# Kernel optimization log

Hardware: AMD Instinct MI355X
Metric: run time of the kernel (lower is better)

The kernel has to match this reference:

```python
import jax, jax.numpy as jnp
import numpy as np

N_NODES = 100000
N_EDGES = 1600000
D_IN = 128
D_HID = 128
N_CLS = 16
N_GRAPHS = 64


def setup_inputs() -> dict:
    key = jax.random.key(0)
    ks = jax.random.split(key, 12)
    h = jax.random.normal(ks[0], (N_NODES, D_IN), dtype=jnp.float32)
    src = jax.random.randint(ks[1], (N_EDGES,), 0, N_NODES, dtype=jnp.int32)
    dst = jax.random.randint(ks[2], (N_EDGES,), 0, N_NODES, dtype=jnp.int32)
    graph_ids = jnp.sort(jax.random.randint(ks[3], (N_NODES,), 0, N_GRAPHS, dtype=jnp.int32))
    s = 1.0 / np.sqrt(D_IN)
    W1_self = jax.random.uniform(ks[4], (D_IN, D_HID), jnp.float32, -s, s)
    W1_neigh = jax.random.uniform(ks[5], (D_IN, D_HID), jnp.float32, -s, s)
    b1 = jnp.zeros((D_HID,), jnp.float32)
    s2 = 1.0 / np.sqrt(D_HID)
    W2_self = jax.random.uniform(ks[6], (D_HID, D_HID), jnp.float32, -s2, s2)
    W2_neigh = jax.random.uniform(ks[7], (D_HID, D_HID), jnp.float32, -s2, s2)
    b2 = jnp.zeros((D_HID,), jnp.float32)
    Wc = jax.random.uniform(ks[8], (D_HID, N_CLS), jnp.float32, -s2, s2)
    bc = jnp.zeros((N_CLS,), jnp.float32)
    return {"h": h, "src": src, "dst": dst, "graph_ids": graph_ids, "num_graphs": N_GRAPHS,
            "W1_self": W1_self, "W1_neigh": W1_neigh, "b1": b1,
            "W2_self": W2_self, "W2_neigh": W2_neigh, "b2": b2,
            "Wc": Wc, "bc": bc}


def _sage_conv(h, src, dst, W_self, W_neigh, b):
    # DGL SAGEConv 'mean': out = fc_self(h) + fc_neigh(mean of in-neighbor feats) + bias
    n = h.shape[0]
    msg = jnp.take(h, src, axis=0)                               # [E, d] gather
    agg = jax.ops.segment_sum(msg, dst, num_segments=n)          # [N, d] scatter-add
    deg = jax.ops.segment_sum(jnp.ones((src.shape[0],), h.dtype), dst, num_segments=n)
    neigh = agg / jnp.maximum(deg, 1.0)[:, None]                 # mean, zero-degree safe
    return h @ W_self + neigh @ W_neigh + b


def reference(h, src, dst, graph_ids, num_graphs,
              W1_self, W1_neigh, b1, W2_self, W2_neigh, b2, Wc, bc):
    x = jax.nn.relu(_sage_conv(h, src, dst, W1_self, W1_neigh, b1))
    x = _sage_conv(x, src, dst, W2_self, W2_neigh, b2)
    # dgl.mean_nodes: per-graph mean over node features
    gsum = jax.ops.segment_sum(x, graph_ids, num_segments=num_graphs)    # [G, d]
    gcnt = jax.ops.segment_sum(jnp.ones((x.shape[0],), x.dtype), graph_ids, num_segments=num_graphs)
    hg = gsum / jnp.maximum(gcnt, 1.0)[:, None]
    return hg @ Wc + bc                                                  # [G, num_classes]
```

## Files before the change

### kernel.cpp

```cpp
#include <hip/hip_runtime.h>

#define D        128
#define N_GRAPHS 64
#define N_CLS    16
#define LDA      40
#define SLOTS    48
#define CAP      8192

typedef unsigned int   uint;
typedef unsigned short ushort;
typedef __attribute__((ext_vector_type(8))) short short8;
typedef __attribute__((ext_vector_type(4))) float f32x4;

__device__ inline ushort f2b(float f) {
    uint u = __float_as_uint(f);
    u += 0x7fffu + ((u >> 16) & 1u);
    return (ushort)(u >> 16);
}


__global__ __launch_bounds__(256) void k_part(
    const int* __restrict__ src, const int* __restrict__ dst,
    int* __restrict__ bcount, uint* __restrict__ ebuf, int E, int NB) {
    __shared__ int hist[512], base[512], lcur[512];
    int t = threadIdx.x;
    int per = (E + gridDim.x - 1) / gridDim.x;
    int e0 = blockIdx.x * per;
    int e1 = min(e0 + per, E);
    for (int i = t; i < NB; i += 256) { hist[i] = 0; lcur[i] = 0; }
    __syncthreads();
    for (int e = e0 + t; e < e1; e += 256) atomicAdd(&hist[dst[e] >> 8], 1);
    __syncthreads();
    for (int i = t; i < NB; i += 256)
        base[i] = hist[i] ? atomicAdd(&bcount[i], hist[i]) : 0;
    __syncthreads();
    for (int e = e0 + t; e < e1; e += 256) {
        int dd = dst[e];
        int b = dd >> 8;
        int off = atomicAdd(&lcur[b], 1);
        int pos = base[b] + off;
        if (pos < CAP)
            ebuf[(size_t)b * CAP + pos] = ((uint)src[e] << 8) | (uint)(dd & 255);
    }
}


__global__ __launch_bounds__(1024) void k_bucket(
    const uint* __restrict__ ebuf, const int* __restrict__ bcount,
    int* __restrict__ csrf, int* __restrict__ deg, float* __restrict__ invdeg,
    int N) {
    __shared__ int ldeg[256];
    __shared__ int lcsr[256 * SLOTS];
    int b = blockIdx.x, t = threadIdx.x;
    if (t < 256) ldeg[t] = 0;
    __syncthreads();
    int cnt = bcount[b];
    if (cnt > CAP) cnt = CAP;
    const uint* __restrict__ eb = ebuf + (size_t)b * CAP;
    for (int i = t; i < cnt; i += 1024) {
        uint r = eb[i];
        int dl = r & 255;
        int sl = atomicAdd(&ldeg[dl], 1);
        if (sl < SLOTS) lcsr[dl * SLOTS + sl] = (int)(r >> 8);
    }
    __syncthreads();
    int n0 = b << 8;
    int lim = (N - n0) * SLOTS;
    if (lim > 256 * SLOTS) lim = 256 * SLOTS;
    for (int i = t; i < lim; i += 1024)
        csrf[(size_t)n0 * SLOTS + i] = lcsr[i];
    if (t < 256 && n0 + t < N) {
        int d = ldeg[t];
        deg[n0 + t] = d;
        invdeg[n0 + t] = 1.0f / (float)(d > 1 ? d : 1);
    }
}

__global__ void k_gbound(const int* __restrict__ gid, int* __restrict__ gstart, int N) {
    int g = threadIdx.x;
    if (g > N_GRAPHS) return;
    int lo = 0, hi = N;
    while (lo < hi) {
        int mid = (lo + hi) >> 1;
        if (gid[mid] < g) lo = mid + 1; else hi = mid;
    }
    gstart[g] = lo;
}


__global__ void k_cast(const float* __restrict__ x, ushort* __restrict__ y, int total4) {
    int i = blockIdx.x * 256 + threadIdx.x;
    if (i < total4) {
        float4 v = ((const float4*)x)[i];
        ushort4 o;
        o.x = f2b(v.x); o.y = f2b(v.y); o.z = f2b(v.z); o.w = f2b(v.w);
        ((ushort4*)y)[i] = o;
    }
}

__global__ void k_castw(const float* __restrict__ Ws, const float* __restrict__ Wn,
                        ushort* __restrict__ wT) {
    int i = blockIdx.x * 256 + threadIdx.x;
    int c = i >> 8, k = i & 255;
    float v = (k < 128) ? Ws[k * 128 + c] : Wn[(k - 128) * 128 + c];
    wT[c * 256 + k] = f2b(v);
}


__global__ __launch_bounds__(256) void k_aggb(
    const ushort* __restrict__ fb, const int* __restrict__ deg,
    const int* __restrict__ csrf, const float* __restrict__ invdeg,
    ushort* __restrict__ outb, int N) {
    int lane = threadIdx.x & 63;
    int n = blockIdx.x * 4 + (threadIdx.x >> 6);
    if (n >= N) return;
    int d = deg[n];
    if (d > SLOTS) d = SLOTS;
    const int* __restrict__ lst = csrf + (size_t)n * SLOTS;
    int ej = lane >> 4;
    int cg = lane & 15;

    float acc[8];
#pragma unroll
    for (int i = 0; i < 8; i++) acc[i] = 0.f;

    int e = ej;
    for (; e + 4 < d; e += 8) {
        int s0 = lst[e];
        int s1 = lst[e + 4];
        uint4 v0 = *(const uint4*)(fb + (size_t)s0 * D + cg * 8);
        uint4 v1 = *(const uint4*)(fb + (size_t)s1 * D + cg * 8);
        acc[0] += __uint_as_float(v0.x << 16);
        acc[1] += __uint_as_float(v0.x & 0xffff0000u);
        acc[2] += __uint_as_float(v0.y << 16);
        acc[3] += __uint_as_float(v0.y & 0xffff0000u);
        acc[4] += __uint_as_float(v0.z << 16);
        acc[5] += __uint_as_float(v0.z & 0xffff0000u);
        acc[6] += __uint_as_float(v0.w << 16);
        acc[7] += __uint_as_float(v0.w & 0xffff0000u);
        acc[0] += __uint_as_float(v1.x << 16);
        acc[1] += __uint_as_float(v1.x & 0xffff0000u);
        acc[2] += __uint_as_float(v1.y << 16);
        acc[3] += __uint_as_float(v1.y & 0xffff0000u);
        acc[4] += __uint_as_float(v1.z << 16);
        acc[5] += __uint_as_float(v1.z & 0xffff0000u);
        acc[6] += __uint_as_float(v1.w << 16);
        acc[7] += __uint_as_float(v1.w & 0xffff0000u);
    }
    for (; e < d; e += 4) {
        int s = lst[e];
        uint4 v = *(const uint4*)(fb + (size_t)s * D + cg * 8);
        acc[0] += __uint_as_float(v.x << 16);
        acc[1] += __uint_as_float(v.x & 0xffff0000u);
        acc[2] += __uint_as_float(v.y << 16);
        acc[3] += __uint_as_float(v.y & 0xffff0000u);
        acc[4] += __uint_as_float(v.z << 16);
        acc[5] += __uint_as_float(v.z & 0xffff0000u);
        acc[6] += __uint_as_float(v.w << 16);
        acc[7] += __uint_as_float(v.w & 0xffff0000u);
    }
#pragma unroll
    for (int i = 0; i < 8; i++) {
        acc[i] += __shfl_xor(acc[i], 16);
        acc[i] += __shfl_xor(acc[i], 32);
    }
    if (ej == 0) {
        float id = invdeg[n];
        uint4 o;
        o.x = (uint)f2b(acc[0] * id) | ((uint)f2b(acc[1] * id) << 16);
        o.y = (uint)f2b(acc[2] * id) | ((uint)f2b(acc[3] * id) << 16);
        o.z = (uint)f2b(acc[4] * id) | ((uint)f2b(acc[5] * id) << 16);
        o.w = (uint)f2b(acc[6] * id) | ((uint)f2b(acc[7] * id) << 16);
        *(uint4*)(outb + (size_t)n * D + cg * 8) = o;
    }
}


__global__ __launch_bounds__(256, 2) void k_mm1m(
    const ushort* __restrict__ hb, const ushort* __restrict__ nbb,
    const ushort* __restrict__ wT, const float* __restrict__ b,
    ushort* __restrict__ x1b, int N) {
    __shared__ __align__(16) ushort As[128 * LDA];
    __shared__ __align__(16) ushort Bs[128 * LDA];
    int t    = threadIdx.x;
    int w    = t >> 6;
    int lane = t & 63;
    int m    = lane & 15;
    int quad = lane >> 4;
    int n0   = blockIdx.x * 128;

    f32x4 acc[2][8];
#pragma unroll
    for (int rt = 0; rt < 2; rt++)
#pragma unroll
        for (int ct = 0; ct < 8; ct++) acc[rt][ct] = (f32x4){0.f, 0.f, 0.f, 0.f};

#pragma unroll 1
    for (int kc = 0; kc < 8; kc++) {
        int k0 = kc * 32;
        const ushort* __restrict__ A = (k0 < 128) ? hb : nbb;
        int ka = k0 & 127;
        __syncthreads();
#pragma unroll
        for (int i = 0; i < 2; i++) {
            int linear = i * 256 + t;
            int row = linear >> 2;
            int q   = linear & 3;
            int nn = n0 + row;
            uint4 v = make_uint4(0u, 0u, 0u, 0u);
            if (nn < N) v = *(const uint4*)(A + (size_t)nn * D + ka + q * 8);
            *(uint4*)(&As[row * LDA + q * 8]) = v;
        }
#pragma unroll
        for (int i = 0; i < 2; i++) {
            int linear = i * 256 + t;
            int col = linear >> 2;
            int q   = linear & 3;
            uint4 v = *(const uint4*)(wT + (size_t)col * 256 + k0 + q * 8);
            *(uint4*)(&Bs[col * LDA + q * 8]) = v;
        }
        __syncthreads();
        short8 af[2], bf[8];
#pragma unroll
        for (int rt = 0; rt < 2; rt++)
            af[rt] = *(const short8*)(&As[(w * 32 + rt * 16 + m) * LDA + quad * 8]);
#pragma unroll
        for (int ct = 0; ct < 8; ct++)
            bf[ct] = *(const short8*)(&Bs[(ct * 16 + m) * LDA + quad * 8]);
#pragma unroll
        for (int rt = 0; rt < 2; rt++)
#pragma unroll
            for (int ct = 0; ct < 8; ct++)
                acc[rt][ct] = __builtin_amdgcn_mfma_f32_16x16x32_bf16(
                    af[rt], bf[ct], acc[rt][ct], 0, 0, 0);
    }
#pragma unroll
    for (int ct = 0; ct < 8; ct++) {
        float bias = b[ct * 16 + m];
#pragma unroll
        for (int rt = 0; rt < 2; rt++) {
#pragma unroll
            for (int r = 0; r < 4; r++) {
                int n = n0 + w * 32 + rt * 16 + quad * 4 + r;
                if (n < N)
                    x1b[(size_t)n * D + ct * 16 + m] =
                        f2b(fmaxf(acc[rt][ct][r] + bias, 0.f));
            }
        }
    }
}


__global__ __launch_bounds__(256) void k_gsum(
    const ushort* __restrict__ x1b, const ushort* __restrict__ n2b,
    const int* __restrict__ gstart, float* __restrict__ S1,
    float* __restrict__ S2) {
    int g  = blockIdx.x >> 3;
    int ch = blockIdx.x & 7;
    int r0 = gstart[g], r1 = gstart[g + 1];
    int len = r1 - r0;
    if (len <= 0) return;
    int L = (len + 7) >> 3;
    int a = r0 + ch * L;
    int bnd = min(a + L, r1);
    if (a >= bnd) return;

    int tid = threadIdx.x;
    int mat = tid >> 7;
    int rp  = (tid >> 6) & 1;
    int cp  = tid & 63;
    const ushort* __restrict__ M = mat ? n2b : x1b;
    float ax = 0.f, ay = 0.f;
    for (int n = a + rp; n < bnd; n += 2) {
        uint v = *(const uint*)(M + (size_t)n * D + cp * 2);
        ax += __uint_as_float(v << 16);
        ay += __uint_as_float(v & 0xffff0000u);
    }
    float* __restrict__ S = mat ? S2 : S1;
    atomicAdd(&S[g * D + cp * 2], ax);
    atomicAdd(&S[g * D + cp * 2 + 1], ay);
}


__global__ void k_final(const float* __restrict__ S1, const float* __restrict__ S2,
                        const int* __restrict__ gstart, const float* __restrict__ W2s,
                        const float* __restrict__ W2n, const float* __restrict__ b2,
                        const float* __restrict__ Wc, const float* __restrict__ bc,
                        float* __restrict__ out) {
    __shared__ float s1[D], s2[D], hg[D];
    int g = blockIdx.x, c = threadIdx.x;
    s1[c] = S1[g * D + c];
    s2[c] = S2[g * D + c];
    __syncthreads();
    float acc = 0.f;
#pragma unroll 8
    for (int k = 0; k < D; k++) {
        acc = fmaf(s1[k], W2s[k * D + c], acc);
        acc = fmaf(s2[k], W2n[k * D + c], acc);
    }
    int cnt = gstart[g + 1] - gstart[g];
    hg[c] = (cnt > 0) ? (acc / (float)cnt + b2[c]) : 0.f;
    __syncthreads();
    if (c < N_CLS) {
        float o = bc[c];
        for (int k = 0; k < D; k++) o = fmaf(hg[k], Wc[k * N_CLS + c], o);
        out[g * N_CLS + c] = o;
    }
}


extern "C" void kernel_launch(void* const* d_in, const int* in_sizes, int n_in,
                              void* d_out, int out_size, void* d_ws, size_t ws_size,
                              hipStream_t stream) {
    const float* h   = (const float*)d_in[0];
    const int*   src = (const int*)d_in[1];
    const int*   dst = (const int*)d_in[2];
    const int*   gid = (const int*)d_in[3];
    const float* W1s = (const float*)d_in[5];
    const float* W1n = (const float*)d_in[6];
    const float* b1  = (const float*)d_in[7];
    const float* W2s = (const float*)d_in[8];
    const float* W2n = (const float*)d_in[9];
    const float* b2  = (const float*)d_in[10];
    const float* Wc  = (const float*)d_in[11];
    const float* bc  = (const float*)d_in[12];
    float* out = (float*)d_out;

    const int N = in_sizes[0] / D;
    const int E = in_sizes[1];
    const int NB = (N + 255) >> 8;

    char* w = (char*)d_ws;
    size_t off = 0;
    auto alloc = [&](size_t elems) -> void* {
        void* p = w + off;
        off += elems * 4;
        return p;
    };
    float* S1     = (float*)alloc((size_t)N_GRAPHS * D);
    float* S2     = (float*)alloc((size_t)N_GRAPHS * D);
    int*   bcount = (int*)alloc(512);
    size_t zero_bytes = off;
    int*   deg    = (int*)alloc(N);
    float* invdeg = (float*)alloc(N);
    int*   gstart = (int*)alloc(128);
    int*   csrf   = (int*)alloc((size_t)N * SLOTS);
    ushort* fb    = (ushort*)alloc((size_t)N * 64);
    ushort* nbb   = (ushort*)alloc((size_t)N * 64);
    ushort* x1b   = (ushort*)alloc((size_t)N * 64);
    ushort* wT    = (ushort*)alloc(16384);
    uint* ebuf = (uint*)nbb;
    (void)ws_size;

    hipMemsetAsync(d_ws, 0, zero_bytes, stream);

    int nbk = (N + 255) / 256;
    int t4  = N * 32;

    k_cast<<<(t4 + 255) / 256, 256, 0, stream>>>(h, fb, t4);
    k_castw<<<128, 256, 0, stream>>>(W1s, W1n, wT);
    k_part<<<256, 256, 0, stream>>>(src, dst, bcount, ebuf, E, NB);
    k_bucket<<<NB, 1024, 0, stream>>>(ebuf, bcount, csrf, deg, invdeg, N);
    k_gbound<<<1, 128, 0, stream>>>(gid, gstart, N);
    k_aggb<<<(N + 3) / 4, 256, 0, stream>>>(fb, deg, csrf, invdeg, nbb, N);
    k_mm1m<<<(N + 127) / 128, 256, 0, stream>>>(fb, nbb, wT, b1, x1b, N);
    k_aggb<<<(N + 3) / 4, 256, 0, stream>>>(x1b, deg, csrf, invdeg, nbb, N);
    k_gsum<<<N_GRAPHS * 8, 256, 0, stream>>>(x1b, nbb, gstart, S1, S2);
    k_final<<<N_GRAPHS, 128, 0, stream>>>(S1, S2, gstart, W2s, W2n, b2, Wc, bc, out);
    (void)nbk;
}
```

Before: 355.0 us.

## Replace second-layer neighbor aggregation with per-source graph coefficient weighted sums

```diff
diff --git a/kernel.cpp b/kernel.cpp
--- a/kernel.cpp
+++ b/kernel.cpp
@@ -6,6 +6,7 @@
 #define LDA      40
 #define SLOTS    48
 #define CAP      8192
+#define NCH      768
 
 typedef unsigned int   uint;
 typedef unsigned short ushort;
@@ -251,10 +252,75 @@
 }
 
 
-__global__ __launch_bounds__(256) void k_gsum(
-    const ushort* __restrict__ x1b, const ushort* __restrict__ n2b,
-    const int* __restrict__ gstart, float* __restrict__ S1,
-    float* __restrict__ S2) {
+__global__ __launch_bounds__(256) void k_wcoef(
+    const int* __restrict__ src, const int* __restrict__ dst,
+    const int* __restrict__ gid, const float* __restrict__ invdeg,
+    float* __restrict__ wc, int E) {
+    int i = blockIdx.x * 256 + threadIdx.x;
+    if (i >= E) return;
+    int s = src[i];
+    int d = dst[i];
+    atomicAdd(&wc[(size_t)s * 64 + gid[d]], invdeg[d]);
+}
+
+__global__ __launch_bounds__(256) void k_s2(
+    const float* __restrict__ wc, const ushort* __restrict__ x1b,
+    float* __restrict__ P, int N) {
+    __shared__ float wl[4][64];
+    __shared__ uint  xl[4][64];
+    const uint* __restrict__ x1u = (const uint*)x1b;
+    int t  = threadIdx.x;
+    int gq = t >> 6;
+    int cp = t & 63;
+    int chunk = blockIdx.x;
+    int a = (int)(((long long)chunk * N) / NCH);
+    int b = (int)(((long long)(chunk + 1) * N) / NCH);
+
+    float acc[16][2];
+#pragma unroll
+    for (int g = 0; g < 16; g++) { acc[g][0] = 0.f; acc[g][1] = 0.f; }
+
+    for (int n0 = a; n0 < b; n0 += 4) {
+        int n = n0 + gq;
+        bool ok = n < b;
+        wl[gq][cp] = ok ? wc[(size_t)n * 64 + cp] : 0.f;
+        xl[gq][cp] = ok ? x1u[(size_t)n * 64 + cp] : 0u;
+        __syncthreads();
+#pragma unroll
+        for (int nn = 0; nn < 4; nn++) {
+            uint xv = xl[nn][cp];
+            float x0 = __uint_as_float(xv << 16);
+            float x1 = __uint_as_float(xv & 0xffff0000u);
+#pragma unroll
+            for (int gg = 0; gg < 16; gg++) {
+                float wv = wl[nn][gq * 16 + gg];
+                acc[gg][0] = fmaf(wv, x0, acc[gg][0]);
+                acc[gg][1] = fmaf(wv, x1, acc[gg][1]);
+            }
+        }
+        __syncthreads();
+    }
+    float2* __restrict__ Pp = (float2*)(P + (size_t)chunk * 8192);
+#pragma unroll
+    for (int gg = 0; gg < 16; gg++)
+        Pp[(gq * 16 + gg) * 64 + cp] = make_float2(acc[gg][0], acc[gg][1]);
+}
+
+__global__ __launch_bounds__(256) void k_s2red(
+    const float* __restrict__ P, float* __restrict__ S2) {
+    int i = blockIdx.x * 256 + threadIdx.x;
+    int c0 = blockIdx.y * (NCH / 8);
+    float s = 0.f;
+#pragma unroll 8
+    for (int ch = 0; ch < NCH / 8; ch++)
+        s += P[(size_t)(c0 + ch) * 8192 + i];
+    atomicAdd(&S2[i], s);
+}
+
+
+__global__ __launch_bounds__(256) void k_gsum1(
+    const ushort* __restrict__ x1b, const int* __restrict__ gstart,
+    float* __restrict__ S1) {
     int g  = blockIdx.x >> 3;
     int ch = blockIdx.x & 7;
     int r0 = gstart[g], r1 = gstart[g + 1];
@@ -265,20 +331,17 @@
     int bnd = min(a + L, r1);
     if (a >= bnd) return;
 
-    int tid = threadIdx.x;
-    int mat = tid >> 7;
-    int rp  = (tid >> 6) & 1;
-    int cp  = tid & 63;
-    const ushort* __restrict__ M = mat ? n2b : x1b;
+    int rp = threadIdx.x >> 6;
+    int cp = threadIdx.x & 63;
     float ax = 0.f, ay = 0.f;
-    for (int n = a + rp; n < bnd; n += 2) {
-        uint v = *(const uint*)(M + (size_t)n * D + cp * 2);
+    const uint* __restrict__ M = (const uint*)x1b;
+    for (int n = a + rp; n < bnd; n += 4) {
+        uint v = M[(size_t)n * 64 + cp];
         ax += __uint_as_float(v << 16);
         ay += __uint_as_float(v & 0xffff0000u);
     }
-    float* __restrict__ S = mat ? S2 : S1;
-    atomicAdd(&S[g * D + cp * 2], ax);
-    atomicAdd(&S[g * D + cp * 2 + 1], ay);
+    atomicAdd(&S1[g * D + cp * 2], ax);
+    atomicAdd(&S1[g * D + cp * 2 + 1], ay);
 }
 
 
@@ -349,12 +412,13 @@
     ushort* nbb   = (ushort*)alloc((size_t)N * 64);
     ushort* x1b   = (ushort*)alloc((size_t)N * 64);
     ushort* wT    = (ushort*)alloc(16384);
-    uint* ebuf = (uint*)nbb;
-    (void)ws_size;
+    uint*  ebuf  = (uint*)nbb;
+    float* wcoef = (float*)fb;
+    float* P     = (float*)nbb;
+    (void)ws_size; (void)csrf;
 
     hipMemsetAsync(d_ws, 0, zero_bytes, stream);
 
-    int nbk = (N + 255) / 256;
     int t4  = N * 32;
 
     k_cast<<<(t4 + 255) / 256, 256, 0, stream>>>(h, fb, t4);
@@ -364,8 +428,10 @@
     k_gbound<<<1, 128, 0, stream>>>(gid, gstart, N);
     k_aggb<<<(N + 3) / 4, 256, 0, stream>>>(fb, deg, csrf, invdeg, nbb, N);
     k_mm1m<<<(N + 127) / 128, 256, 0, stream>>>(fb, nbb, wT, b1, x1b, N);
-    k_aggb<<<(N + 3) / 4, 256, 0, stream>>>(x1b, deg, csrf, invdeg, nbb, N);
-    k_gsum<<<N_GRAPHS * 8, 256, 0, stream>>>(x1b, nbb, gstart, S1, S2);
+    hipMemsetAsync(wcoef, 0, (size_t)N * 64 * sizeof(float), stream);
+    k_wcoef<<<(E + 255) / 256, 256, 0, stream>>>(src, dst, gid, invdeg, wcoef, E);
+    k_s2<<<NCH, 256, 0, stream>>>(wcoef, x1b, P, N);
+    k_s2red<<<dim3(32, 8), 256, 0, stream>>>(P, S2);
+    k_gsum1<<<N_GRAPHS * 8, 256, 0, stream>>>(x1b, gstart, S1);
     k_final<<<N_GRAPHS, 128, 0, stream>>>(S1, S2, gstart, W2s, W2n, b2, Wc, bc, out);
-    (void)nbk;
-}
+}
```

Result: slower. 411.5 us (+15.9%).
